# Kernel optimization log

Measured on AMD Instinct MI355X. Metric: run time of the kernel, lower is better.

The kernel has to match this reference:

```python
import jax, jax.numpy as jnp
import numpy as np
from jax.scipy.special import xlogy

B, P, L, V = 32, 64, 64, 32000
TEMP = 1.0            # temperature == init_temp at call time
DSUB = DINS = DDEL = 1.0
EPS = 1e-13


def setup_inputs() -> dict:
    key = jax.random.key(0)
    k1, k2, k3, k4 = jax.random.split(key, 4)
    # outputs are log-probabilities (input to KLDivLoss)
    outputs = jax.nn.log_softmax(jax.random.normal(k1, (B, P, V), jnp.float32), axis=-1)
    output_symbols = jax.random.randint(k2, (B, P), 0, V, dtype=jnp.int32)
    targets = jax.random.randint(k3, (B, L), 0, V, dtype=jnp.int32)
    lengths = jax.random.randint(k4, (B,), L // 2, L + 1)
    mask = jnp.arange(L)[None, :] < lengths[:, None]   # (B, L) bool
    return {"outputs": outputs, "output_symbols": output_symbols,
            "targets": targets, "mask": mask}


def _edit_distance(output_symbols, targets, mask):
    """Wavefront (row-scan) edit-distance DP. Returns (B, P, L) float32.

    Row recurrence: d[i,j] = min(d[i-1,j-1] + dsub*neq, d[i-1,j] + dins,
                                 d[i,j-1] + ddel).
    The intra-row dependence (d[i,j-1] + ddel) is a min-plus prefix scan:
    d[i,j] = ddel*j + cummin_k<=j(tmp[k] - ddel*k), with tmp = min(diag, ins).
    """
    Bv, Pv = output_symbols.shape
    Lv = targets.shape[1]
    row0 = jnp.broadcast_to(jnp.arange(Lv, dtype=jnp.float32), (Bv, Lv))
    offs = DDEL * jnp.arange(Lv, dtype=jnp.float32)

    def step(prev, xs):
        i, sym = xs                                    # i: scalar, sym: (B,)
        neq = (sym[:, None] != targets[:, :-1]).astype(jnp.float32)  # (B, L-1)
        tmp = jnp.minimum(prev[:, :-1] + DSUB * neq,   # diagonal
                          prev[:, 1:] + DINS)          # insertion
        tmp = jnp.concatenate([jnp.full((Bv, 1), i, jnp.float32), tmp], axis=1)
        cur = offs + jax.lax.cummin(tmp - offs, axis=1)  # deletion prefix-min
        return cur, cur

    ivals = jnp.arange(1, Pv, dtype=jnp.float32)
    syms = output_symbols[:, :-1].T                    # (P-1, B)
    _, rows = jax.lax.scan(step, row0, (ivals, syms))
    dist = jnp.concatenate([row0[None], rows], axis=0).transpose(1, 0, 2)
    return jnp.where(mask[:, None, :], dist, jnp.inf)


def _q_values(outputs, output_symbols, targets, mask):
    dist = _edit_distance(output_symbols, targets, mask)     # (B, P, L)
    min_d = dist.min(axis=-1)                                # (B, P)
    truth = (dist == min_d[..., None]).astype(outputs.dtype) # (B, P, L)
    b_idx = jnp.arange(B)[:, None, None]
    i_idx = jnp.arange(P)[None, :, None]
    t_idx = jnp.broadcast_to(targets[:, None, :], (B, P, L))
    # scatter: q[b, i, targets[b, j]] = 1 wherever truth[b, i, j]
    q = jnp.zeros((B, P, V), outputs.dtype).at[b_idx, i_idx, t_idx].max(truth)
    return q - (1.0 + min_d)[..., None]


def reference(outputs, output_symbols, targets, mask):
    mask = mask.astype(bool)
    q = _q_values(outputs, output_symbols, targets, mask)
    optimal_policy = jax.nn.softmax(q / TEMP, axis=-1)
    # KLDivLoss(reduction='none'): p * (log p - input), 0 where p == 0
    kl = xlogy(optimal_policy, optimal_policy) - optimal_policy * outputs
    loss = kl.sum(axis=-1) * mask.astype(jnp.float32)        # (B, P)
    wsum = mask.astype(jnp.float32).sum(axis=-1)             # (B,)
    per_batch = loss.sum(axis=-1) / (wsum + EPS)
    n_nonempty = (wsum > 0).astype(jnp.float32).sum() + EPS
    return per_batch.sum() / n_nonempty
```

## Files before the change

kernel.cpp:

```cpp
#include <hip/hip_runtime.h>
#include <cstdint>
#include <cstddef>

#define Bn 32
#define Pn 64
#define Ln 64
#define Vn 32000

__global__ __launch_bounds__(256) void edocd_dp(
    const int* __restrict__ syms,
    const int* __restrict__ targets,
    const void* __restrict__ maskp,
    unsigned long long* __restrict__ dedup,
    float* __restrict__ wvec,
    float* __restrict__ wsum_out,
    float* __restrict__ d_out)
{
    const int b    = blockIdx.x;
    const int tid  = threadIdx.x;
    const int wave = tid >> 6;
    const int lane = tid & 63;

    __shared__ float dist[Pn * Ln];
    __shared__ int   tg[Ln];
    __shared__ unsigned long long mbits_sh;

    if (tid < Ln) tg[tid] = targets[b * Ln + tid];
    __syncthreads();

    if (wave == 0) {
        const unsigned char* m8 = (const unsigned char*)maskp;
        const bool is_u8 = (m8[1] != 0);
        const bool mj = is_u8 ? (m8[b * Ln + lane] != 0)
                              : (((const int*)maskp)[b * Ln + lane] != 0);
        const unsigned long long mbits = __ballot(mj);
        const float ws = (float)__popcll(mbits);
        if (lane == 0) {
            wsum_out[b] = ws;
            mbits_sh    = mbits;
            if (b == 0) d_out[0] = 0.0f;
        }
        wvec[b * Pn + lane] = mj ? (1.0f / (ws + 1e-13f)) : 0.0f;

        const int i   = lane;
        const int sym = (i >= 1) ? syms[b * Pn + i - 1] : -1;
        float a1 = 0.0f;
        float a2 = 0.0f;
        for (int k = 0; k < Pn + Ln - 1; ++k) {
            const float up = __shfl_up(a1, 1);
            const float ud = __shfl_up(a2, 1);
            const int j = k - i;
            float val = a1;
            if (j >= 0 && j < Ln) {
                if (i == 0)      val = (float)j;
                else if (j == 0) val = (float)i;
                else {
                    const float neq = (sym != tg[j - 1]) ? 1.0f : 0.0f;
                    val = fminf(ud + neq, fminf(up, a1) + 1.0f);
                }
                dist[i * Ln + j] = val;
            }
            a2 = a1;
            a1 = val;
        }
    }
    __syncthreads();

    const unsigned long long mbits = mbits_sh;
    const bool mj = (mbits >> lane) & 1ull;
    const unsigned long long earlier_mask =
        (lane == 0) ? 0ull : (~0ull >> (64 - lane));
    const int tself = tg[lane];

    for (int r = 0; r < 16; ++r) {
        const int i = wave * 16 + r;
        const float cur = dist[i * Ln + lane];
        float mn = mj ? cur : INFINITY;
        #pragma unroll
        for (int d = 32; d >= 1; d >>= 1) mn = fminf(mn, __shfl_xor(mn, d));

        bool opt = mj && (cur == mn);
        const unsigned long long bits = __ballot(opt);
        if (opt) {
            unsigned long long e = bits & earlier_mask;
            while (e) {
                const int kk = __ffsll((unsigned long long)e) - 1;
                e &= e - 1;
                if (tg[kk] == tself) { opt = false; break; }
            }
        }
        const unsigned long long dm = __ballot(opt);
        if (lane == 0) dedup[b * Pn + i] = dm;
    }
}

__global__ __launch_bounds__(256) void edocd_kl(
    const float* __restrict__ outputs,
    const int* __restrict__ targets,
    const unsigned long long* __restrict__ dedup,
    const float* __restrict__ wvec,
    const float* __restrict__ wsum_in,
    float* __restrict__ d_out)
{
    const int id   = blockIdx.x;
    const int b    = id >> 6;
    const int tid  = threadIdx.x;
    const int wave = tid >> 6, lane = tid & 63;

    const float* __restrict__ row = outputs + (size_t)id * Vn;
    const float4* __restrict__ row4 = (const float4*)row;

    float p0 = 0.0f, p1 = 0.0f, p2 = 0.0f, p3 = 0.0f;
    int idx = tid;
    for (; idx + 768 < Vn / 4; idx += 1024) {
        const float4 va = row4[idx];
        const float4 vb = row4[idx + 256];
        const float4 vc = row4[idx + 512];
        const float4 vd = row4[idx + 768];
        p0 += (va.x + va.y) + (va.z + va.w);
        p1 += (vb.x + vb.y) + (vb.z + vb.w);
        p2 += (vc.x + vc.y) + (vc.z + vc.w);
        p3 += (vd.x + vd.y) + (vd.z + vd.w);
    }
    for (; idx < Vn / 4; idx += 256) {
        const float4 v = row4[idx];
        p0 += (v.x + v.y) + (v.z + v.w);
    }
    float partial = (p0 + p1) + (p2 + p3);
    #pragma unroll
    for (int d = 32; d >= 1; d >>= 1) partial += __shfl_xor(partial, d);

    __shared__ float red[4];
    __shared__ float sopt_sh;
    if (lane == 0) red[wave] = partial;

    const unsigned long long M = dedup[id];
    if (wave == 0) {
        float so = 0.0f;
        if ((M >> lane) & 1ull) so = row[targets[b * Ln + lane]];
        #pragma unroll
        for (int d = 32; d >= 1; d >>= 1) so += __shfl_xor(so, d);
        if (lane == 0) sopt_sh = so;
    }
    __syncthreads();

    if (tid == 0) {
        const float w = wvec[id];
        if (w != 0.0f) {
            const float S_all = (red[0] + red[1]) + (red[2] + red[3]);
            const float S_opt = sopt_sh;
            const float m = (float)__popcll(M);

            float cnt = 0.0f;
            #pragma unroll
            for (int bb = 0; bb < Bn; ++bb)
                cnt += (wsum_in[bb] > 0.0f) ? 1.0f : 0.0f;
            const float nn = cnt + 1e-13f;

            const float einv = 0.36787944117144233f;
            const float D    = m + ((float)Vn - m) * einv;
            const float p_hi = 1.0f / D;
            const float p_lo = einv / D;

            const float plogp = m * p_hi * logf(p_hi)
                              + ((float)Vn - m) * p_lo * logf(p_lo);
            const float cross = p_lo * S_all + (p_hi - p_lo) * S_opt;
            const float kl = plogp - cross;

            atomicAdd(d_out, kl * w / nn);
        }
    }
}

extern "C" void kernel_launch(void* const* d_in, const int* in_sizes, int n_in,
                              void* d_out, int out_size, void* d_ws, size_t ws_size,
                              hipStream_t stream)
{
    const float* outputs = (const float*)d_in[0];
    const int*   syms    = (const int*)d_in[1];
    const int*   targets = (const int*)d_in[2];
    const void*  mask    = d_in[3];

    float* out = (float*)d_out;
    char*  ws  = (char*)d_ws;

    unsigned long long* dedup = (unsigned long long*)ws;
    float* wvec = (float*)(ws + 16384);
    float* wsum = (float*)(ws + 16384 + 8192);

    edocd_dp<<<Bn, 256, 0, stream>>>(syms, targets, mask, dedup, wvec, wsum, out);
    edocd_kl<<<Bn * Pn, 256, 0, stream>>>(outputs, targets, dedup, wvec, wsum, out);
}
```

Measured before the change: 449.7 us.

## Fuse edit-distance DP into KL kernel, one launch with warp specialization

Merges the DP kernel and the KL reduction kernel into a single launch of B*P blocks. Wave 0 of each block recomputes the full edit-distance DP for its batch and derives its row's dedup mask, while waves 1-3 stream the outputs row to sum it. This removes the second launch, the workspace round trip and the serialization between the two kernels, at the cost of repeating the DP 64 times per batch and reading the row with three waves instead of four. A memset replaces the in-kernel zeroing of the output.

```diff
diff --git a/kernel.cpp b/kernel.cpp
--- a/kernel.cpp
+++ b/kernel.cpp
@@ -7,155 +7,117 @@
 #define Ln 64
 #define Vn 32000
 
-__global__ __launch_bounds__(256) void edocd_dp(
+__global__ __launch_bounds__(256) void edocd_fused(
+    const float* __restrict__ outputs,
     const int* __restrict__ syms,
     const int* __restrict__ targets,
     const void* __restrict__ maskp,
-    unsigned long long* __restrict__ dedup,
-    float* __restrict__ wvec,
-    float* __restrict__ wsum_out,
     float* __restrict__ d_out)
 {
-    const int b    = blockIdx.x;
+    const int id   = blockIdx.x;
+    const int b    = id >> 6;
+    const int i    = id & 63;
     const int tid  = threadIdx.x;
     const int wave = tid >> 6;
     const int lane = tid & 63;
 
     __shared__ float dist[Pn * Ln];
     __shared__ int   tg[Ln];
-    __shared__ unsigned long long mbits_sh;
+    __shared__ float red[3];
 
-    if (tid < Ln) tg[tid] = targets[b * Ln + tid];
+    if (wave != 0) {
+        const float4* __restrict__ row4 =
+            (const float4*)(outputs + (size_t)id * Vn);
+        const int t = tid - 64;
+        float p0 = 0.0f, p1 = 0.0f;
+        int idx = t;
+        for (; idx + 192 < Vn / 4; idx += 384) {
+            const float4 a = row4[idx];
+            const float4 c = row4[idx + 192];
+            p0 += (a.x + a.y) + (a.z + a.w);
+            p1 += (c.x + c.y) + (c.z + c.w);
+        }
+        if (idx < Vn / 4) {
+            const float4 a = row4[idx];
+            p0 += (a.x + a.y) + (a.z + a.w);
+        }
+        float partial = p0 + p1;
+        #pragma unroll
+        for (int d = 32; d >= 1; d >>= 1) partial += __shfl_xor(partial, d);
+        if (lane == 0) red[wave - 1] = partial;
+        __syncthreads();
+        return;
+    }
+
+    const float* __restrict__ row = outputs + (size_t)id * Vn;
+
+    tg[lane] = targets[b * Ln + lane];
+
+    const unsigned char* m8 = (const unsigned char*)maskp;
+    const bool is_u8 = (m8[1] != 0);
+    const bool mj = is_u8 ? (m8[b * Ln + lane] != 0)
+                          : (((const int*)maskp)[b * Ln + lane] != 0);
+    const unsigned long long mbits = __ballot(mj);
+    const float ws = (float)__popcll(mbits);
+
+    bool nz = false;
+    if (lane < Bn)
+        nz = is_u8 ? (m8[lane * Ln] != 0)
+                   : (((const int*)maskp)[lane * Ln] != 0);
+    const float nn = (float)__popcll(__ballot(nz)) + 1e-13f;
+
+    const int sym = (lane >= 1) ? syms[b * Pn + lane - 1] : -1;
+    float a1 = 0.0f, a2 = 0.0f;
+    for (int k = 0; k < Pn + Ln - 1; ++k) {
+        const float up = __shfl_up(a1, 1);
+        const float ud = __shfl_up(a2, 1);
+        const int j = k - lane;
+        float val = a1;
+        if (j >= 0 && j < Ln) {
+            if (lane == 0)   val = (float)j;
+            else if (j == 0) val = (float)lane;
+            else {
+                const float neq = (sym != tg[j - 1]) ? 1.0f : 0.0f;
+                val = fminf(ud + neq, fminf(up, a1) + 1.0f);
+            }
+            dist[lane * Ln + j] = val;
+        }
+        a2 = a1;
+        a1 = val;
+    }
+
+    const float cur = dist[i * Ln + lane];
+    float mn = mj ? cur : INFINITY;
+    #pragma unroll
+    for (int d = 32; d >= 1; d >>= 1) mn = fminf(mn, __shfl_xor(mn, d));
+
+    bool opt = mj && (cur == mn);
+    const unsigned long long bits = __ballot(opt);
+    if (opt) {
+        const int tself = tg[lane];
+        unsigned long long e =
+            bits & ((lane == 0) ? 0ull : (~0ull >> (64 - lane)));
+        while (e) {
+            const int kk = __ffsll((unsigned long long)e) - 1;
+            e &= e - 1;
+            if (tg[kk] == tself) { opt = false; break; }
+        }
+    }
+    const unsigned long long M = __ballot(opt);
+
+    float so = 0.0f;
+    if ((M >> lane) & 1ull) so = row[tg[lane]];
+    #pragma unroll
+    for (int d = 32; d >= 1; d >>= 1) so += __shfl_xor(so, d);
+
     __syncthreads();
 
-    if (wave == 0) {
-        const unsigned char* m8 = (const unsigned char*)maskp;
-        const bool is_u8 = (m8[1] != 0);
-        const bool mj = is_u8 ? (m8[b * Ln + lane] != 0)
-                              : (((const int*)maskp)[b * Ln + lane] != 0);
-        const unsigned long long mbits = __ballot(mj);
-        const float ws = (float)__popcll(mbits);
-        if (lane == 0) {
-            wsum_out[b] = ws;
-            mbits_sh    = mbits;
-            if (b == 0) d_out[0] = 0.0f;
-        }
-        wvec[b * Pn + lane] = mj ? (1.0f / (ws + 1e-13f)) : 0.0f;
-
-        const int i   = lane;
-        const int sym = (i >= 1) ? syms[b * Pn + i - 1] : -1;
-        float a1 = 0.0f;
-        float a2 = 0.0f;
-        for (int k = 0; k < Pn + Ln - 1; ++k) {
-            const float up = __shfl_up(a1, 1);
-            const float ud = __shfl_up(a2, 1);
-            const int j = k - i;
-            float val = a1;
-            if (j >= 0 && j < Ln) {
-                if (i == 0)      val = (float)j;
-                else if (j == 0) val = (float)i;
-                else {
-                    const float neq = (sym != tg[j - 1]) ? 1.0f : 0.0f;
-                    val = fminf(ud + neq, fminf(up, a1) + 1.0f);
-                }
-                dist[i * Ln + j] = val;
-            }
-            a2 = a1;
-            a1 = val;
-        }
-    }
-    __syncthreads();
-
-    const unsigned long long mbits = mbits_sh;
-    const bool mj = (mbits >> lane) & 1ull;
-    const unsigned long long earlier_mask =
-        (lane == 0) ? 0ull : (~0ull >> (64 - lane));
-    const int tself = tg[lane];
-
-    for (int r = 0; r < 16; ++r) {
-        const int i = wave * 16 + r;
-        const float cur = dist[i * Ln + lane];
-        float mn = mj ? cur : INFINITY;
-        #pragma unroll
-        for (int d = 32; d >= 1; d >>= 1) mn = fminf(mn, __shfl_xor(mn, d));
-
-        bool opt = mj && (cur == mn);
-        const unsigned long long bits = __ballot(opt);
-        if (opt) {
-            unsigned long long e = bits & earlier_mask;
-            while (e) {
-                const int kk = __ffsll((unsigned long long)e) - 1;
-                e &= e - 1;
-                if (tg[kk] == tself) { opt = false; break; }
-            }
-        }
-        const unsigned long long dm = __ballot(opt);
-        if (lane == 0) dedup[b * Pn + i] = dm;
-    }
-}
-
-__global__ __launch_bounds__(256) void edocd_kl(
-    const float* __restrict__ outputs,
-    const int* __restrict__ targets,
-    const unsigned long long* __restrict__ dedup,
-    const float* __restrict__ wvec,
-    const float* __restrict__ wsum_in,
-    float* __restrict__ d_out)
-{
-    const int id   = blockIdx.x;
-    const int b    = id >> 6;
-    const int tid  = threadIdx.x;
-    const int wave = tid >> 6, lane = tid & 63;
-
-    const float* __restrict__ row = outputs + (size_t)id * Vn;
-    const float4* __restrict__ row4 = (const float4*)row;
-
-    float p0 = 0.0f, p1 = 0.0f, p2 = 0.0f, p3 = 0.0f;
-    int idx = tid;
-    for (; idx + 768 < Vn / 4; idx += 1024) {
-        const float4 va = row4[idx];
-        const float4 vb = row4[idx + 256];
-        const float4 vc = row4[idx + 512];
-        const float4 vd = row4[idx + 768];
-        p0 += (va.x + va.y) + (va.z + va.w);
-        p1 += (vb.x + vb.y) + (vb.z + vb.w);
-        p2 += (vc.x + vc.y) + (vc.z + vc.w);
-        p3 += (vd.x + vd.y) + (vd.z + vd.w);
-    }
-    for (; idx < Vn / 4; idx += 256) {
-        const float4 v = row4[idx];
-        p0 += (v.x + v.y) + (v.z + v.w);
-    }
-    float partial = (p0 + p1) + (p2 + p3);
-    #pragma unroll
-    for (int d = 32; d >= 1; d >>= 1) partial += __shfl_xor(partial, d);
-
-    __shared__ float red[4];
-    __shared__ float sopt_sh;
-    if (lane == 0) red[wave] = partial;
-
-    const unsigned long long M = dedup[id];
-    if (wave == 0) {
-        float so = 0.0f;
-        if ((M >> lane) & 1ull) so = row[targets[b * Ln + lane]];
-        #pragma unroll
-        for (int d = 32; d >= 1; d >>= 1) so += __shfl_xor(so, d);
-        if (lane == 0) sopt_sh = so;
-    }
-    __syncthreads();
-
-    if (tid == 0) {
-        const float w = wvec[id];
-        if (w != 0.0f) {
-            const float S_all = (red[0] + red[1]) + (red[2] + red[3]);
-            const float S_opt = sopt_sh;
-            const float m = (float)__popcll(M);
-
-            float cnt = 0.0f;
-            #pragma unroll
-            for (int bb = 0; bb < Bn; ++bb)
-                cnt += (wsum_in[bb] > 0.0f) ? 1.0f : 0.0f;
-            const float nn = cnt + 1e-13f;
+    if (lane == 0) {
+        const bool mi = (mbits >> i) & 1ull;
+        if (mi) {
+            const float w     = 1.0f / (ws + 1e-13f);
+            const float S_all = red[0] + red[1] + red[2];
+            const float m     = (float)__popcll(M);
 
             const float einv = 0.36787944117144233f;
             const float D    = m + ((float)Vn - m) * einv;
@@ -164,7 +126,7 @@
 
             const float plogp = m * p_hi * logf(p_hi)
                               + ((float)Vn - m) * p_lo * logf(p_lo);
-            const float cross = p_lo * S_all + (p_hi - p_lo) * S_opt;
+            const float cross = p_lo * S_all + (p_hi - p_lo) * so;
             const float kl = plogp - cross;
 
             atomicAdd(d_out, kl * w / nn);
@@ -181,13 +143,7 @@
     const int*   targets = (const int*)d_in[2];
     const void*  mask    = d_in[3];
 
-    float* out = (float*)d_out;
-    char*  ws  = (char*)d_ws;
-
-    unsigned long long* dedup = (unsigned long long*)ws;
-    float* wvec = (float*)(ws + 16384);
-    float* wsum = (float*)(ws + 16384 + 8192);
-
-    edocd_dp<<<Bn, 256, 0, stream>>>(syms, targets, mask, dedup, wvec, wsum, out);
-    edocd_kl<<<Bn * Pn, 256, 0, stream>>>(outputs, targets, dedup, wvec, wsum, out);
+    hipMemsetAsync(d_out, 0, sizeof(float), stream);
+    edocd_fused<<<Bn * Pn, 256, 0, stream>>>(outputs, syms, targets, mask,
+                                             (float*)d_out);
 }
```

New measurement: 363.2 us (median of 2 runs). 1.24x faster.
